# Kernel optimization log

Measured on AMD Instinct MI355X. Metric: run time of the kernel, lower is better.

Reference implementation:

```python
import jax, jax.numpy as jnp
import numpy as np

B, N, C, H, D, K = 4, 8192, 384, 12, 2, 256
M = N // K          # 32 members per cluster
CH = C // H         # 32 head dim


def setup_inputs() -> dict:
    key = jax.random.key(0)
    ks = jax.random.split(key, 8)
    pos = jax.random.uniform(ks[0], (B, N, D), jnp.float32) * 100.0
    feat = jax.random.normal(ks[1], (B, N, C), jnp.float32)
    # each batch's points partitioned into K clusters of M members (a permutation)
    perms = jax.vmap(lambda kk: jax.random.permutation(kk, N))(jax.random.split(ks[2], B))
    member_idx = perms.reshape(B * K, M).astype(jnp.int32)               # z x m
    batch_idx = jnp.broadcast_to(
        jnp.repeat(jnp.arange(B, dtype=jnp.int32), K)[:, None], (B * K, M))
    w = 0.02
    qkv_w = jax.random.normal(ks[3], (3 * C, C), jnp.float32) * w
    qkv_b = jnp.zeros((3 * C,), jnp.float32)
    pos_w = jax.random.normal(ks[4], (H, D), jnp.float32) * w
    pos_b = jnp.zeros((H,), jnp.float32)
    proj_w = jax.random.normal(ks[5], (C, C), jnp.float32) * w
    proj_b = jnp.zeros((C,), jnp.float32)
    return dict(pos=pos, feat=feat, member_idx=member_idx, batch_idx=batch_idx,
                qkv_w=qkv_w, qkv_b=qkv_b, pos_w=pos_w, pos_b=pos_b,
                proj_w=proj_w, proj_b=proj_b, k=K)


def reference(pos, feat, member_idx, batch_idx, qkv_w, qkv_b, pos_w, pos_b,
              proj_w, proj_b, k):
    # attend_means=True, mask=None, cluster_score=None, q_subsample_idx=None path
    b, n, c = feat.shape
    d = pos.shape[2]
    h = pos_w.shape[0]
    ch = c // h
    z, m = member_idx.shape
    scale = ch ** -0.5

    qkv = feat @ qkv_w.T + qkv_b            # b,n,3c
    q = qkv[..., :c]                        # b,n,c
    kv = qkv[..., c:]                       # b,n,2c

    pos_orig = pos
    pos_n = pos / jnp.max(pos.reshape(-1, d), axis=0)   # per-coordinate max norm

    # irregular gather of kv / pos per cluster member
    kv_g = kv[batch_idx, member_idx]        # z,m,2c
    pos_g = pos_n[batch_idx, member_idx]    # z,m,d

    # cluster_score=None, mask=None -> uniform weights 1/m (mean over members)
    kv_mean = jnp.mean(kv_g, axis=1).reshape(b, k, 2, h, ch)
    pos_mean = jnp.mean(pos_g, axis=1).reshape(b, k, d)

    key_ = kv_mean[:, :, 0].transpose(0, 2, 1, 3)   # b,h,k,ch
    v = kv_mean[:, :, 1].transpose(0, 2, 1, 3)      # b,h,k,ch
    qh = q.reshape(b, n, h, ch).transpose(0, 2, 1, 3) * scale  # b,h,n,ch

    attn = jnp.einsum('bhnc,bhkc->bhnk', qh, key_)  # b,h,n,k
    rel_pos = pos_mean[:, None, :, :] - pos_orig[:, :, None, :]  # b,n,k,d
    pos_bias = jnp.einsum('bnkd,hd->bhnk', rel_pos, pos_w) + pos_b[None, :, None, None]
    attn = jax.nn.softmax(attn + pos_bias, axis=-1)

    out = jnp.einsum('bhnk,bhkc->bnhc', attn, v).reshape(b, n, c)
    return out @ proj_w.T + proj_b
```

## Files before the change

kernel.cpp:

```cpp
#include <hip/hip_runtime.h>

typedef __attribute__((ext_vector_type(8))) short bf16x8;
typedef __attribute__((ext_vector_type(4))) float f32x4;

#define MFMA16(a,b,c) __builtin_amdgcn_mfma_f32_16x16x32_bf16((a),(b),(c),0,0,0)

__device__ __forceinline__ float b2f(unsigned short u){
  union { unsigned u; float f; } x; x.u = ((unsigned)u) << 16; return x.f;
}
__device__ __forceinline__ unsigned short f2b(float f){
  union { float f; unsigned u; } x; x.f = f;
  unsigned r = x.u + 0x7FFFu + ((x.u >> 16) & 1u);
  return (unsigned short)(r >> 16);
}
__device__ __forceinline__ unsigned pk_rne(float a, float b){
  unsigned ua = __float_as_uint(a), ub = __float_as_uint(b);
  ua += 0x7FFFu + ((ua >> 16) & 1u);
  ub += 0x7FFFu + ((ub >> 16) & 1u);
  return __builtin_amdgcn_perm(ub, ua, 0x07060302u);
}
__device__ __forceinline__ unsigned pk_trunc(float a, float b){
  return __builtin_amdgcn_perm(__float_as_uint(b), __float_as_uint(a), 0x07060302u);
}
__device__ __forceinline__ bf16x8 mk8(unsigned a, unsigned b, unsigned c, unsigned d){
  union { uint4 u; bf16x8 h; } x; x.u = make_uint4(a,b,c,d); return x.h;
}
__device__ __forceinline__ int permp(int cl){
  return (cl & 0xE0) | (((cl >> 2) & 3) << 3) | (((cl >> 4) & 1) << 2) | (cl & 3);
}

typedef __attribute__((address_space(3))) unsigned int lds_u32;
typedef const __attribute__((address_space(1))) unsigned int glb_u32;
__device__ __forceinline__ void gl_lds16(const void* g, void* l){
  __builtin_amdgcn_global_load_lds((glb_u32*)g, (lds_u32*)l, 16, 0, 0);
}

__global__ __launch_bounds__(192) void prep_means_kernel(
    const float* __restrict__ pos, unsigned* __restrict__ pmax,
    const float* __restrict__ qkv_w, unsigned short* __restrict__ qkvwb,
    const float* __restrict__ proj_w, unsigned short* __restrict__ projwb,
    const float* __restrict__ feat,
    const int* __restrict__ member_idx, const int* __restrict__ batch_idx,
    unsigned short* __restrict__ fm, float* __restrict__ pm,
    unsigned short* __restrict__ featb)
{
  int bid = blockIdx.x, t = threadIdx.x;
  if (bid < 1024){
    int g = t / 96, tl = t - g*96;
    int z = bid;
    __shared__ int bases[32];
    __shared__ float4 part[96];
    if (t < 32) bases[t] = batch_idx[z*32 + t]*8192 + member_idx[z*32 + t];
    __syncthreads();
    if (t < 32){
      float2 pp = ((const float2*)pos)[bases[t]];
      #pragma unroll
      for (int off = 16; off >= 1; off >>= 1){
        pp.x += __shfl_xor(pp.x, off, 32);
        pp.y += __shfl_xor(pp.y, off, 32);
      }
      if (t == 0){ pm[z*2] = pp.x*(1.f/32.f); pm[z*2+1] = pp.y*(1.f/32.f); }
    }
    float4 v[16]; int rows[16];
    const float4* f4 = (const float4*)feat;
    #pragma unroll
    for (int m = 0; m < 16; m++){
      rows[m] = bases[g*16 + m];
      v[m] = f4[(long)rows[m]*96 + tl];
    }
    float4 a = {0.f,0.f,0.f,0.f};
    #pragma unroll
    for (int m = 0; m < 16; m++){
      *(uint2*)(featb + (long)rows[m]*384 + tl*4) =
          make_uint2(pk_rne(v[m].x, v[m].y), pk_rne(v[m].z, v[m].w));
      a.x += v[m].x; a.y += v[m].y; a.z += v[m].z; a.w += v[m].w;
    }
    if (g == 1) part[tl] = a;
    __syncthreads();
    if (g == 0){
      float4 b = part[tl];
      a.x += b.x; a.y += b.y; a.z += b.z; a.w += b.w;
      unsigned d0 = pk_rne(a.x*(1.f/32.f), a.y*(1.f/32.f));
      unsigned d1 = pk_rne(a.z*(1.f/32.f), a.w*(1.f/32.f));
      *(uint2*)(fm + (long)z*384 + tl*4) = make_uint2(d0, d1);
    }
  } else if (bid < 1408){
    int u = (bid - 1024)*192 + t;
    const float* in; unsigned short* o; long i;
    if (u < 55296){ in = qkv_w;  o = qkvwb;  i = u; }
    else          { in = proj_w; o = projwb; i = u - 55296; }
    const float4* p = (const float4*)(in + i*8);
    float4 a = p[0], b = p[1];
    *(uint4*)(o + i*8) = make_uint4(pk_rne(a.x,a.y), pk_rne(a.z,a.w),
                                    pk_rne(b.x,b.y), pk_rne(b.z,b.w));
  } else {
    int i = (bid - 1408)*192 + t;
    if (i < 16384){
      float4 v = ((const float4*)pos)[i];
      float m0 = fmaxf(v.x, v.z), m1 = fmaxf(v.y, v.w);
      #pragma unroll
      for (int off = 32; off >= 1; off >>= 1){
        m0 = fmaxf(m0, __shfl_xor(m0, off, 64));
        m1 = fmaxf(m1, __shfl_xor(m1, off, 64));
      }
      if ((t & 63) == 0){
        atomicMax(&pmax[0], __float_as_uint(m0));
        atomicMax(&pmax[1], __float_as_uint(m1));
      }
    }
  }
}

__global__ __launch_bounds__(512) void kvq_kernel(
    const unsigned short* __restrict__ fm,
    const unsigned short* __restrict__ featb,
    const unsigned short* __restrict__ qkvwb,
    const float* __restrict__ qkv_b,
    const float* __restrict__ pm, const float* __restrict__ pmaxf,
    const float* __restrict__ pos_w, const float* __restrict__ pos_b,
    unsigned short* __restrict__ kh, unsigned short* __restrict__ vt,
    unsigned short* __restrict__ wt,
    unsigned short* __restrict__ q_s, float q_scale)
{
  __shared__ unsigned short As[64*64];
  __shared__ unsigned short Ws[384*64];
  __shared__ unsigned short wtS[256];
  const int K = 384;
  int tid = threadIdx.x;
  int lane = tid & 63, wave = tid >> 6;
  int l15 = lane & 15, quad = lane >> 4;
  int sw = l15 & 7;
  int srow = tid >> 3, sc8 = tid & 7;

  int qtile;
  if (blockIdx.x < 96){
    int mt = blockIdx.x / 6, nt = blockIdx.x - mt*6;
    int m0 = mt << 6, n0 = nt << 7;
    int b = m0 >> 8, cl0 = m0 & 255;
    const unsigned short* W = qkvwb + 384*384;
    if (nt >= 3 && tid < 256){
      int lh = tid >> 6, lc = tid & 63;
      int h = ((n0 - 384) >> 5) + lh;
      int cl = cl0 + lc;
      float p0 = pm[(b*256 + cl)*2]   / pmaxf[0];
      float p1 = pm[(b*256 + cl)*2+1] / pmaxf[1];
      float bias = p0*pos_w[h*2] + p1*pos_w[h*2+1] + pos_b[h];
      unsigned short wv = f2b(exp2f(bias * 1.44269504088896340f));
      wtS[lh*64 + lc] = wv;
      wt[(((long)(b*12 + h)) << 8) + permp(cl)] = wv;
    }
    int wr = (wave >> 2) << 5, wc = (wave & 3) << 5;
    f32x4 acc[2][2];
    #pragma unroll
    for (int i = 0; i < 2; i++)
      #pragma unroll
      for (int j = 0; j < 2; j++) acc[i][j] = (f32x4){0.f,0.f,0.f,0.f};

    for (int k0 = 0; k0 < K; k0 += 64){
      __syncthreads();
      int gc8 = sc8 ^ (srow & 7);
      gl_lds16(fm + (long)(m0+srow)*K + k0 + gc8*8, As + wave*512);
      #pragma unroll
      for (int it = 0; it < 2; it++){
        int r = it*64 + srow;
        int g2 = sc8 ^ (r & 7);
        gl_lds16(W + (long)(n0+r)*K + k0 + g2*8, Ws + it*4096 + wave*512);
      }
      __syncthreads();
      #pragma unroll
      for (int kk = 0; kk < 2; kk++){
        bf16x8 af[2], bfr[2];
        #pragma unroll
        for (int i = 0; i < 2; i++)
          af[i] = *(const bf16x8*)(As + (wr + i*16 + l15)*64 + (((kk<<2)+quad) ^ sw)*8);
        #pragma unroll
        for (int j = 0; j < 2; j++)
          bfr[j] = *(const bf16x8*)(Ws + (wc + j*16 + l15)*64 + (((kk<<2)+quad) ^ sw)*8);
        #pragma unroll
        for (int i = 0; i < 2; i++)
          #pragma unroll
          for (int j = 0; j < 2; j++)
            acc[i][j] = MFMA16(af[i], bfr[j], acc[i][j]);
      }
    }

    #pragma unroll
    for (int j = 0; j < 2; j++){
      int col = n0 + wc + j*16 + l15;
      float bv = qkv_b[384 + col];
      #pragma unroll
      for (int i = 0; i < 2; i++){
        #pragma unroll
        for (int r = 0; r < 4; r++){
          float v = acc[i][j][r] + bv;
          int lr = wr + i*16 + quad*4 + r;
          int cl = cl0 + lr;
          if (col < 384){
            int h = col >> 5, ch = col & 31;
            kh[((((long)b*12 + h)*256 + cl)*32) + ch] = f2b(v);
          } else {
            int cn = col - 384;
            int h = cn >> 5, ch = cn & 31;
            int pp = permp(cl);
            int c8 = (pp >> 3) ^ (ch & 7);
            float w = b2f(wtS[(wave & 3)*64 + lr]);
            vt[(((long)b*12 + h)*32 + ch)*256 + c8*8 + (pp & 7)] = f2b(v * w);
          }
        }
      }
    }
    qtile = 416 + blockIdx.x;
  } else {
    qtile = blockIdx.x - 96;
  }

  {
    int m0 = qtile << 6;
    f32x4 acc[4][3];
    #pragma unroll
    for (int i = 0; i < 4; i++)
      #pragma unroll
      for (int j = 0; j < 3; j++) acc[i][j] = (f32x4){0.f,0.f,0.f,0.f};

    for (int k0 = 0; k0 < K; k0 += 64){
      __syncthreads();
      int gc8 = sc8 ^ (srow & 7);
      gl_lds16(featb + (long)(m0+srow)*K + k0 + gc8*8, As + wave*512);
      #pragma unroll
      for (int it = 0; it < 6; it++){
        int r = it*64 + srow;
        int g2 = sc8 ^ (r & 7);
        gl_lds16(qkvwb + (long)r*K + k0 + g2*8, Ws + it*4096 + wave*512);
      }
      __syncthreads();
      #pragma unroll
      for (int kk = 0; kk < 2; kk++){
        bf16x8 af[4];
        #pragma unroll
        for (int i = 0; i < 4; i++)
          af[i] = *(const bf16x8*)(As + (i*16 + l15)*64 + (((kk<<2)+quad) ^ sw)*8);
        #pragma unroll
        for (int j = 0; j < 3; j++){
          bf16x8 bfr = *(const bf16x8*)(Ws + (wave*48 + j*16 + l15)*64 + (((kk<<2)+quad) ^ sw)*8);
          #pragma unroll
          for (int i = 0; i < 4; i++)
            acc[i][j] = MFMA16(af[i], bfr, acc[i][j]);
        }
      }
    }

    #pragma unroll
    for (int j = 0; j < 3; j++){
      int col = wave*48 + j*16 + l15;
      float bv = qkv_b[col];
      #pragma unroll
      for (int i = 0; i < 4; i++){
        int row0 = m0 + i*16 + quad*4;
        #pragma unroll
        for (int r = 0; r < 4; r++){
          float v = (acc[i][j][r] + bv) * q_scale;
          int row = row0 + r;
          int bb = row >> 13, tok = row & 8191;
          q_s[((((long)(bb*12 + (col >> 5))) << 13) + tok)*32 + (col & 31)] = f2b(v);
        }
      }
    }
  }
}

__global__ __launch_bounds__(512, 4) void attnproj_kernel(
    const unsigned short* __restrict__ qhm,
    const unsigned short* __restrict__ kh,
    const unsigned short* __restrict__ vt,
    const unsigned short* __restrict__ wt,
    const unsigned short* __restrict__ projwb,
    const float* __restrict__ proj_b,
    float* __restrict__ out)
{
  __shared__ unsigned short keyS[16384];
  __shared__ unsigned short vTS[16384];
  __shared__ unsigned short oS[64*64];
  __shared__ unsigned short wS[512];

  int bid = blockIdx.x;
  int b = bid >> 7;
  int t0 = (bid & 127) << 6;
  int tid = threadIdx.x, lane = tid & 63, wave = tid >> 6;
  int l15 = lane & 15, quad = lane >> 4;
  int sw = l15 & 7;
  int hsel = wave >> 2, ti = wave & 3;

  f32x4 acc[4][3];
  #pragma unroll
  for (int i = 0; i < 4; i++)
    #pragma unroll
    for (int j = 0; j < 3; j++) acc[i][j] = (f32x4){0.f,0.f,0.f,0.f};

  for (int it = 0; it < 6; it++){
    int h0 = 2*it;
    const unsigned short* ks = kh + ((long)b*12 + h0)*8192;
    const unsigned short* vs = vt + ((long)b*12 + h0)*8192;
    #pragma unroll
    for (int p = 0; p < 4; p++){
      gl_lds16(ks + p*4096 + tid*8, keyS + p*4096 + wave*512);
      gl_lds16(vs + p*4096 + tid*8, vTS  + p*4096 + wave*512);
    }
    if (wave == 0)
      gl_lds16(wt + ((long)b*12 + h0)*256 + lane*8, wS);

    long bh = (long)b*12 + h0 + hsel;
    bf16x8 aq = *(const bf16x8*)(qhm + (bh*8192 + t0 + ti*16 + l15)*32 + quad*8);
    __syncthreads();

    const unsigned short* kb = keyS + hsel*8192;
    const unsigned short* vb = vTS  + hsel*8192;
    const unsigned short* wb = wS   + hsel*256;

    f32x4 o0 = {0.f,0.f,0.f,0.f}, o1 = {0.f,0.f,0.f,0.f}, os = {0.f,0.f,0.f,0.f};
    #pragma unroll
    for (int ks8 = 0; ks8 < 8; ks8++){
      bf16x8 bk0 = *(const bf16x8*)(kb + ((2*ks8  )*16 + l15)*32 + quad*8);
      bf16x8 bk1 = *(const bf16x8*)(kb + ((2*ks8+1)*16 + l15)*32 + quad*8);
      const f32x4 z4 = {0.f,0.f,0.f,0.f};
      f32x4 s0 = MFMA16(bk0, aq, z4);
      f32x4 s1 = MFMA16(bk1, aq, z4);
      #pragma unroll
      for (int c = 0; c < 4; c++){ s0[c] = exp2f(s0[c]); s1[c] = exp2f(s1[c]); }
      bf16x8 pf = mk8(pk_trunc(s0[0],s0[1]), pk_trunc(s0[2],s0[3]),
                      pk_trunc(s1[0],s1[1]), pk_trunc(s1[2],s1[3]));
      int c8 = (4*ks8 + quad) ^ sw;
      bf16x8 a0 = *(const bf16x8*)(vb + l15*256      + c8*8);
      bf16x8 a1 = *(const bf16x8*)(vb + (16+l15)*256 + c8*8);
      bf16x8 wf = *(const bf16x8*)(wb + ks8*32 + quad*8);
      o0 = MFMA16(a0, pf, o0);
      o1 = MFMA16(a1, pf, o1);
      os = MFMA16(wf, pf, os);
    }

    float inv = 1.f / os[0];
    int tokLoc = ti*16 + l15;
    int oct0 = hsel*4 + (quad >> 1);
    int wi = (quad & 1)*4;
    *(uint2*)(oS + tokLoc*64 + ((oct0 ^ sw)*8 + wi)) =
        make_uint2(pk_rne(o0[0]*inv, o0[1]*inv), pk_rne(o0[2]*inv, o0[3]*inv));
    *(uint2*)(oS + tokLoc*64 + (((oct0+2) ^ sw)*8 + wi)) =
        make_uint2(pk_rne(o1[0]*inv, o1[1]*inv), pk_rne(o1[2]*inv, o1[3]*inv));
    __syncthreads();

    #pragma unroll
    for (int kk = 0; kk < 2; kk++){
      bf16x8 af[4];
      #pragma unroll
      for (int i = 0; i < 4; i++)
        af[i] = *(const bf16x8*)(oS + (i*16 + l15)*64 + (((kk<<2)+quad) ^ sw)*8);
      #pragma unroll
      for (int j = 0; j < 3; j++){
        bf16x8 bfr = *(const bf16x8*)(projwb + (long)(wave*48 + j*16 + l15)*384
                                      + it*64 + (kk*4 + quad)*8);
        #pragma unroll
        for (int i = 0; i < 4; i++)
          acc[i][j] = MFMA16(af[i], bfr, acc[i][j]);
      }
    }
  }

  #pragma unroll
  for (int j = 0; j < 3; j++){
    int col = wave*48 + j*16 + l15;
    float bv = proj_b[col];
    #pragma unroll
    for (int i = 0; i < 4; i++){
      long row0 = (long)b*8192 + t0 + i*16 + quad*4;
      #pragma unroll
      for (int r = 0; r < 4; r++)
        out[(row0 + r)*384 + col] = acc[i][j][r] + bv;
    }
  }
}

extern "C" void kernel_launch(void* const* d_in, const int* in_sizes, int n_in,
                              void* d_out, int out_size, void* d_ws, size_t ws_size,
                              hipStream_t stream)
{
  const float* pos      = (const float*)d_in[0];
  const float* feat     = (const float*)d_in[1];
  const int* member_idx = (const int*)d_in[2];
  const int* batch_idx  = (const int*)d_in[3];
  const float* qkv_w    = (const float*)d_in[4];
  const float* qkv_b    = (const float*)d_in[5];
  const float* pos_w    = (const float*)d_in[6];
  const float* pos_b    = (const float*)d_in[7];
  const float* proj_w   = (const float*)d_in[8];
  const float* proj_b   = (const float*)d_in[9];
  float* out = (float*)d_out;

  char* ws = (char*)d_ws;
  float* pmax           = (float*)ws;
  float* pm             = (float*)(ws + 256);
  unsigned short* fm    = (unsigned short*)(ws + 8704);
  unsigned short* kh    = (unsigned short*)(ws + 795136);
  unsigned short* vt    = (unsigned short*)(ws + 1581568);
  unsigned short* wt    = (unsigned short*)(ws + 2368000);
  unsigned short* q_s   = (unsigned short*)(ws + 2417152);
  unsigned short* qkvwb = (unsigned short*)(ws + 52748800);
  unsigned short* projwb= (unsigned short*)(ws + 53633536);
  unsigned short* featb = (unsigned short*)(ws + 53928448);

  hipMemsetAsync(pmax, 0, 8, stream);
  prep_means_kernel<<<1494, 192, 0, stream>>>(pos, (unsigned*)pmax, qkv_w, qkvwb,
                                              proj_w, projwb, feat, member_idx,
                                              batch_idx, fm, pm, featb);
  kvq_kernel<<<512, 512, 0, stream>>>(fm, featb, qkvwb, qkv_b, pm, pmax, pos_w, pos_b,
                                      kh, vt, wt, q_s,
                                      0.17677669529663687f * 1.44269504088896340f);
  attnproj_kernel<<<512, 512, 0, stream>>>(q_s, kh, vt, wt, projwb, proj_b, out);
}
```

Measured before the change: 186.4 us.

## Double token tile per block in attnproj and swizzle key LDS layout

Each attnproj block now handles 128 tokens instead of 64, so every key/value/weight tile staged in LDS and every projection-weight fragment read from global memory serves twice as many queries, and the grid halves to 256 blocks. The key tile is also stored with an XOR swizzle on its 16-byte chunks to reduce LDS bank conflicts when it is read as MFMA fragments. In exchange the accumulator array doubles (launch bounds lowered to 2 blocks per CU), which raises register pressure. Only 256 blocks are launched, which may leave some compute units idle.

```diff
diff --git a/kernel.cpp b/kernel.cpp
--- a/kernel.cpp
+++ b/kernel.cpp
@@ -268,7 +268,7 @@
   }
 }
 
-__global__ __launch_bounds__(512, 4) void attnproj_kernel(
+__global__ __launch_bounds__(512, 2) void attnproj_kernel(
     const unsigned short* __restrict__ qhm,
     const unsigned short* __restrict__ kh,
     const unsigned short* __restrict__ vt,
@@ -279,20 +279,20 @@
 {
   __shared__ unsigned short keyS[16384];
   __shared__ unsigned short vTS[16384];
-  __shared__ unsigned short oS[64*64];
+  __shared__ unsigned short oS[128*64];
   __shared__ unsigned short wS[512];
 
   int bid = blockIdx.x;
-  int b = bid >> 7;
-  int t0 = (bid & 127) << 6;
+  int b = bid >> 6;
+  int t0 = (bid & 63) << 7;
   int tid = threadIdx.x, lane = tid & 63, wave = tid >> 6;
   int l15 = lane & 15, quad = lane >> 4;
   int sw = l15 & 7;
-  int hsel = wave >> 2, ti = wave & 3;
-
-  f32x4 acc[4][3];
+  int hsel = wave >> 2, w4 = wave & 3;
+
+  f32x4 acc[8][3];
   #pragma unroll
-  for (int i = 0; i < 4; i++)
+  for (int i = 0; i < 8; i++)
     #pragma unroll
     for (int j = 0; j < 3; j++) acc[i][j] = (f32x4){0.f,0.f,0.f,0.f};
 
@@ -302,63 +302,87 @@
     const unsigned short* vs = vt + ((long)b*12 + h0)*8192;
     #pragma unroll
     for (int p = 0; p < 4; p++){
-      gl_lds16(ks + p*4096 + tid*8, keyS + p*4096 + wave*512);
-      gl_lds16(vs + p*4096 + tid*8, vTS  + p*4096 + wave*512);
+      int u = p*512 + wave*64 + lane;
+      int krow = u >> 2;
+      int kc = (u & 3) ^ ((krow >> 1) & 3);
+      gl_lds16(ks + krow*32 + kc*8, keyS + p*4096 + wave*512);
+      gl_lds16(vs + p*4096 + tid*8, vTS + p*4096 + wave*512);
     }
     if (wave == 0)
       gl_lds16(wt + ((long)b*12 + h0)*256 + lane*8, wS);
 
     long bh = (long)b*12 + h0 + hsel;
-    bf16x8 aq = *(const bf16x8*)(qhm + (bh*8192 + t0 + ti*16 + l15)*32 + quad*8);
+    long qb = (bh*8192 + t0 + w4*16 + l15)*32 + quad*8;
+    bf16x8 aq0 = *(const bf16x8*)(qhm + qb);
+    bf16x8 aq1 = *(const bf16x8*)(qhm + qb + 2048);
     __syncthreads();
 
     const unsigned short* kb = keyS + hsel*8192;
     const unsigned short* vb = vTS  + hsel*8192;
     const unsigned short* wb = wS   + hsel*256;
 
-    f32x4 o0 = {0.f,0.f,0.f,0.f}, o1 = {0.f,0.f,0.f,0.f}, os = {0.f,0.f,0.f,0.f};
+    f32x4 o00 = {0.f,0.f,0.f,0.f}, o01 = {0.f,0.f,0.f,0.f}, os0 = {0.f,0.f,0.f,0.f};
+    f32x4 o10 = {0.f,0.f,0.f,0.f}, o11 = {0.f,0.f,0.f,0.f}, os1 = {0.f,0.f,0.f,0.f};
     #pragma unroll
     for (int ks8 = 0; ks8 < 8; ks8++){
-      bf16x8 bk0 = *(const bf16x8*)(kb + ((2*ks8  )*16 + l15)*32 + quad*8);
-      bf16x8 bk1 = *(const bf16x8*)(kb + ((2*ks8+1)*16 + l15)*32 + quad*8);
+      int r0 = 2*ks8*16 + l15;
+      int r1 = r0 + 16;
+      bf16x8 bk0 = *(const bf16x8*)(kb + r0*32 + ((quad ^ ((r0 >> 1) & 3)))*8);
+      bf16x8 bk1 = *(const bf16x8*)(kb + r1*32 + ((quad ^ ((r1 >> 1) & 3)))*8);
       const f32x4 z4 = {0.f,0.f,0.f,0.f};
-      f32x4 s0 = MFMA16(bk0, aq, z4);
-      f32x4 s1 = MFMA16(bk1, aq, z4);
-      #pragma unroll
-      for (int c = 0; c < 4; c++){ s0[c] = exp2f(s0[c]); s1[c] = exp2f(s1[c]); }
-      bf16x8 pf = mk8(pk_trunc(s0[0],s0[1]), pk_trunc(s0[2],s0[3]),
-                      pk_trunc(s1[0],s1[1]), pk_trunc(s1[2],s1[3]));
+      f32x4 s00 = MFMA16(bk0, aq0, z4);
+      f32x4 s01 = MFMA16(bk1, aq0, z4);
+      f32x4 s10 = MFMA16(bk0, aq1, z4);
+      f32x4 s11 = MFMA16(bk1, aq1, z4);
+      #pragma unroll
+      for (int c = 0; c < 4; c++){
+        s00[c] = exp2f(s00[c]); s01[c] = exp2f(s01[c]);
+        s10[c] = exp2f(s10[c]); s11[c] = exp2f(s11[c]);
+      }
+      bf16x8 pf0 = mk8(pk_trunc(s00[0],s00[1]), pk_trunc(s00[2],s00[3]),
+                       pk_trunc(s01[0],s01[1]), pk_trunc(s01[2],s01[3]));
+      bf16x8 pf1 = mk8(pk_trunc(s10[0],s10[1]), pk_trunc(s10[2],s10[3]),
+                       pk_trunc(s11[0],s11[1]), pk_trunc(s11[2],s11[3]));
       int c8 = (4*ks8 + quad) ^ sw;
       bf16x8 a0 = *(const bf16x8*)(vb + l15*256      + c8*8);
       bf16x8 a1 = *(const bf16x8*)(vb + (16+l15)*256 + c8*8);
       bf16x8 wf = *(const bf16x8*)(wb + ks8*32 + quad*8);
-      o0 = MFMA16(a0, pf, o0);
-      o1 = MFMA16(a1, pf, o1);
-      os = MFMA16(wf, pf, os);
-    }
-
-    float inv = 1.f / os[0];
-    int tokLoc = ti*16 + l15;
+      o00 = MFMA16(a0, pf0, o00);
+      o01 = MFMA16(a1, pf0, o01);
+      os0 = MFMA16(wf, pf0, os0);
+      o10 = MFMA16(a0, pf1, o10);
+      o11 = MFMA16(a1, pf1, o11);
+      os1 = MFMA16(wf, pf1, os1);
+    }
+
+    float inv0 = 1.f / os0[0];
+    float inv1 = 1.f / os1[0];
     int oct0 = hsel*4 + (quad >> 1);
     int wi = (quad & 1)*4;
-    *(uint2*)(oS + tokLoc*64 + ((oct0 ^ sw)*8 + wi)) =
-        make_uint2(pk_rne(o0[0]*inv, o0[1]*inv), pk_rne(o0[2]*inv, o0[3]*inv));
-    *(uint2*)(oS + tokLoc*64 + (((oct0+2) ^ sw)*8 + wi)) =
-        make_uint2(pk_rne(o1[0]*inv, o1[1]*inv), pk_rne(o1[2]*inv, o1[3]*inv));
+    int tokLoc0 = w4*16 + l15;
+    *(uint2*)(oS + tokLoc0*64 + ((oct0 ^ sw)*8 + wi)) =
+        make_uint2(pk_rne(o00[0]*inv0, o00[1]*inv0), pk_rne(o00[2]*inv0, o00[3]*inv0));
+    *(uint2*)(oS + tokLoc0*64 + (((oct0+2) ^ sw)*8 + wi)) =
+        make_uint2(pk_rne(o01[0]*inv0, o01[1]*inv0), pk_rne(o01[2]*inv0, o01[3]*inv0));
+    int tokLoc1 = tokLoc0 + 64;
+    *(uint2*)(oS + tokLoc1*64 + ((oct0 ^ sw)*8 + wi)) =
+        make_uint2(pk_rne(o10[0]*inv1, o10[1]*inv1), pk_rne(o10[2]*inv1, o10[3]*inv1));
+    *(uint2*)(oS + tokLoc1*64 + (((oct0+2) ^ sw)*8 + wi)) =
+        make_uint2(pk_rne(o11[0]*inv1, o11[1]*inv1), pk_rne(o11[2]*inv1, o11[3]*inv1));
     __syncthreads();
 
     #pragma unroll
     for (int kk = 0; kk < 2; kk++){
-      bf16x8 af[4];
-      #pragma unroll
-      for (int i = 0; i < 4; i++)
+      bf16x8 af[8];
+      #pragma unroll
+      for (int i = 0; i < 8; i++)
         af[i] = *(const bf16x8*)(oS + (i*16 + l15)*64 + (((kk<<2)+quad) ^ sw)*8);
       #pragma unroll
       for (int j = 0; j < 3; j++){
         bf16x8 bfr = *(const bf16x8*)(projwb + (long)(wave*48 + j*16 + l15)*384
                                       + it*64 + (kk*4 + quad)*8);
         #pragma unroll
-        for (int i = 0; i < 4; i++)
+        for (int i = 0; i < 8; i++)
           acc[i][j] = MFMA16(af[i], bfr, acc[i][j]);
       }
     }
@@ -369,7 +393,7 @@
     int col = wave*48 + j*16 + l15;
     float bv = proj_b[col];
     #pragma unroll
-    for (int i = 0; i < 4; i++){
+    for (int i = 0; i < 8; i++){
       long row0 = (long)b*8192 + t0 + i*16 + quad*4;
       #pragma unroll
       for (int r = 0; r < 4; r++)
@@ -413,5 +437,5 @@
   kvq_kernel<<<512, 512, 0, stream>>>(fm, featb, qkvwb, qkv_b, pm, pmax, pos_w, pos_b,
                                       kh, vt, wt, q_s,
                                       0.17677669529663687f * 1.44269504088896340f);
-  attnproj_kernel<<<512, 512, 0, stream>>>(q_s, kh, vt, wt, projwb, proj_b, out);
-}
+  attnproj_kernel<<<256, 512, 0, stream>>>(q_s, kh, vt, wt, projwb, proj_b, out);
+}
```

New measurement: 193.1 us. 3.6% more time.

## Read key/value tiles directly from global memory and double-buffer oS

Applied to the files above, without the earlier changes.

Drops the per-iteration staging of key, value-transposed and weight tiles into LDS. Each wave now reads these operands straight from global memory, relying on L1/L2 caching. oS becomes double-buffered by iteration parity, so one barrier per iteration is removed. This shrinks LDS from about 73KB to 16KB, which could raise occupancy, but it risks higher global-load latency and redundant traffic. The vb indexing keeps the XOR swizzle c8, which assumes the vt global layout already matches the swizzled LDS layout.

```diff
diff --git a/kernel.cpp b/kernel.cpp
--- a/kernel.cpp
+++ b/kernel.cpp
@@ -277,10 +277,7 @@
     const float* __restrict__ proj_b,
     float* __restrict__ out)
 {
-  __shared__ unsigned short keyS[16384];
-  __shared__ unsigned short vTS[16384];
-  __shared__ unsigned short oS[64*64];
-  __shared__ unsigned short wS[512];
+  __shared__ unsigned short oS[2][64*64];
 
   int bid = blockIdx.x;
   int b = bid >> 7;
@@ -297,30 +294,19 @@
     for (int j = 0; j < 3; j++) acc[i][j] = (f32x4){0.f,0.f,0.f,0.f};
 
   for (int it = 0; it < 6; it++){
-    int h0 = 2*it;
-    const unsigned short* ks = kh + ((long)b*12 + h0)*8192;
-    const unsigned short* vs = vt + ((long)b*12 + h0)*8192;
-    #pragma unroll
-    for (int p = 0; p < 4; p++){
-      gl_lds16(ks + p*4096 + tid*8, keyS + p*4096 + wave*512);
-      gl_lds16(vs + p*4096 + tid*8, vTS  + p*4096 + wave*512);
-    }
-    if (wave == 0)
-      gl_lds16(wt + ((long)b*12 + h0)*256 + lane*8, wS);
-
-    long bh = (long)b*12 + h0 + hsel;
+    int head = 2*it + hsel;
+    long bh = (long)b*12 + head;
+    const unsigned short* kb = kh + bh*8192;
+    const unsigned short* vb = vt + bh*8192;
+    const unsigned short* wb = wt + bh*256;
+
     bf16x8 aq = *(const bf16x8*)(qhm + (bh*8192 + t0 + ti*16 + l15)*32 + quad*8);
-    __syncthreads();
-
-    const unsigned short* kb = keyS + hsel*8192;
-    const unsigned short* vb = vTS  + hsel*8192;
-    const unsigned short* wb = wS   + hsel*256;
 
     f32x4 o0 = {0.f,0.f,0.f,0.f}, o1 = {0.f,0.f,0.f,0.f}, os = {0.f,0.f,0.f,0.f};
     #pragma unroll
     for (int ks8 = 0; ks8 < 8; ks8++){
-      bf16x8 bk0 = *(const bf16x8*)(kb + ((2*ks8  )*16 + l15)*32 + quad*8);
-      bf16x8 bk1 = *(const bf16x8*)(kb + ((2*ks8+1)*16 + l15)*32 + quad*8);
+      bf16x8 bk0 = *(const bf16x8*)(kb + (32*ks8 + l15)*32 + quad*8);
+      bf16x8 bk1 = *(const bf16x8*)(kb + (32*ks8 + 16 + l15)*32 + quad*8);
       const f32x4 z4 = {0.f,0.f,0.f,0.f};
       f32x4 s0 = MFMA16(bk0, aq, z4);
       f32x4 s1 = MFMA16(bk1, aq, z4);
@@ -338,12 +324,13 @@
     }
 
     float inv = 1.f / os[0];
+    unsigned short* ob = &oS[it & 1][0];
     int tokLoc = ti*16 + l15;
     int oct0 = hsel*4 + (quad >> 1);
     int wi = (quad & 1)*4;
-    *(uint2*)(oS + tokLoc*64 + ((oct0 ^ sw)*8 + wi)) =
+    *(uint2*)(ob + tokLoc*64 + ((oct0 ^ sw)*8 + wi)) =
         make_uint2(pk_rne(o0[0]*inv, o0[1]*inv), pk_rne(o0[2]*inv, o0[3]*inv));
-    *(uint2*)(oS + tokLoc*64 + (((oct0+2) ^ sw)*8 + wi)) =
+    *(uint2*)(ob + tokLoc*64 + (((oct0+2) ^ sw)*8 + wi)) =
         make_uint2(pk_rne(o1[0]*inv, o1[1]*inv), pk_rne(o1[2]*inv, o1[3]*inv));
     __syncthreads();
 
@@ -352,7 +339,7 @@
       bf16x8 af[4];
       #pragma unroll
       for (int i = 0; i < 4; i++)
-        af[i] = *(const bf16x8*)(oS + (i*16 + l15)*64 + (((kk<<2)+quad) ^ sw)*8);
+        af[i] = *(const bf16x8*)(ob + (i*16 + l15)*64 + (((kk<<2)+quad) ^ sw)*8);
       #pragma unroll
       for (int j = 0; j < 3; j++){
         bf16x8 bfr = *(const bf16x8*)(projwb + (long)(wave*48 + j*16 + l15)*384
```

Measured after the change: 214.7 us. 1.15x slower.
